# Kernel tuning notes

Hardware: AMD Instinct MI355X
Metric: run time of the kernel (lower is better)

Reference implementation:

```python
import jax, jax.numpy as jnp
import numpy as np

B, D, H1, H2 = 512, 1024, 512, 128

def setup_inputs() -> dict:
    key = jax.random.key(0)
    ks = jax.random.split(key, 3)
    x = jax.random.normal(ks[0], (B, D), dtype=jnp.float32)
    W1 = jax.random.normal(ks[1], (H1, D), dtype=jnp.float32)
    W2 = jax.random.normal(ks[2], (H2, H1), dtype=jnp.float32)
    b1 = jnp.full((H1,), 0.1, dtype=jnp.float32)
    b2 = jnp.full((H2,), 0.1, dtype=jnp.float32)
    b3 = jnp.full((H1,), 0.1, dtype=jnp.float32)
    b_r = jnp.full((D,), 0.1, dtype=jnp.float32)
    return {"x": x, "W1": W1, "b1": b1, "W2": W2, "b2": b2, "b3": b3, "b_r": b_r}

def reference(x, W1, b1, W2, b2, b3, b_r):
    # encoder
    c1 = jax.nn.sigmoid(x @ W1.T + b1)          # [B, H1]
    c2 = jax.nn.sigmoid(c1 @ W2.T + b2)         # [B, H2]
    # decoder (tied weights)
    c3 = jax.nn.sigmoid(c2 @ W2 + b3)           # [B, H1]
    recover = c3 @ W1 + b_r                     # [B, D]
    # Jacobian of code w.r.t. x, batched (replaces per-sample diag+matmul loop):
    # Jac[b] = diag(c2'(b)) @ W2 @ diag(c1'(b)) @ W1
    s1p = c1 * (1.0 - c1)                       # [B, H1]
    s2p = c2 * (1.0 - c2)                       # [B, H2]
    M = s2p[:, :, None] * W2[None, :, :] * s1p[:, None, :]   # [B, H2, H1]
    Jac = jnp.einsum('bhk,kd->bhd', M, W1)      # [B, H2, D]
    return (recover, c2, Jac)
```

## Files before the change

### kernel.cpp

```cpp
#include <hip/hip_runtime.h>


typedef _Float16 f16x8 __attribute__((ext_vector_type(8)));
typedef _Float16 f16x4 __attribute__((ext_vector_type(4)));
typedef float    f32x4 __attribute__((ext_vector_type(4)));
typedef float    f32x2 __attribute__((ext_vector_type(2)));

__device__ __forceinline__ void gld_lds16(const _Float16* src, _Float16* dst_wave_uniform) {
    __builtin_amdgcn_global_load_lds((const __attribute__((address_space(1))) unsigned int*)src,
                                     (__attribute__((address_space(3))) unsigned int*)dst_wave_uniform,
                                     16, 0, 0);
}

__global__ __launch_bounds__(256) void prep_kernel(const float* __restrict__ W1,
                                                   const float* __restrict__ W2,
                                                   _Float16* __restrict__ W1T,
                                                   _Float16* __restrict__ W2h) {
    int bx = blockIdx.x;
    if (bx < 512) {
        __shared__ float tile[32][33];
        int dt = (bx & 31) * 32, kt = (bx >> 5) * 32;
        int tx = threadIdx.x & 31, ty = threadIdx.x >> 5;
        #pragma unroll
        for (int r = 0; r < 32; r += 8)
            tile[ty + r][tx] = W1[(kt + ty + r) * 1024 + dt + tx];
        __syncthreads();
        #pragma unroll
        for (int r = 0; r < 32; r += 8)
            W1T[(size_t)(dt + ty + r) * 512 + kt + tx] = (_Float16)tile[tx][ty + r];
    } else {
        int i = (bx - 512) * 1024 + threadIdx.x * 4;
        f32x4 v = *(const f32x4*)(W2 + i);
        f16x4 h;
        h.x = (_Float16)v.x; h.y = (_Float16)v.y; h.z = (_Float16)v.z; h.w = (_Float16)v.w;
        *(f16x4*)(W2h + i) = h;
    }
}

template <int EPI, bool TRANSB>
__global__ __launch_bounds__(256) void gemm_f32(const float* __restrict__ A,
                                                const float* __restrict__ Bm,
                                                const float* __restrict__ bias,
                                                float* __restrict__ C,
                                                float* __restrict__ Cd,
                                                _Float16* __restrict__ Ch,
                                                int M, int N, int K) {
    __shared__ __align__(16) float As[16][34];
    __shared__ __align__(16) float Bs[16][68];
    const int n0 = blockIdx.x * 64, m0 = blockIdx.y * 32;
    const int tid = threadIdx.x, tx = tid & 15, ty = tid >> 4;
    float acc[2][4] = {};

    for (int k0 = 0; k0 < K; k0 += 16) {
        #pragma unroll
        for (int r = 0; r < 2; ++r) {
            int m = (tid >> 4) + r * 16, k = tid & 15;
            As[k][m] = A[(size_t)(m0 + m) * K + k0 + k];
        }
        if (TRANSB) {
            #pragma unroll
            for (int r = 0; r < 4; ++r) {
                int n = (tid >> 4) + r * 16, k = tid & 15;
                Bs[k][n] = Bm[(size_t)(n0 + n) * K + k0 + k];
            }
        } else {
            #pragma unroll
            for (int r = 0; r < 4; ++r) {
                int k = (tid >> 6) + r * 4, n = tid & 63;
                Bs[k][n] = Bm[(size_t)(k0 + k) * N + n0 + n];
            }
        }
        __syncthreads();
        #pragma unroll
        for (int k = 0; k < 16; ++k) {
            f32x2 av = *(const f32x2*)&As[k][ty * 2];
            f32x4 bv = *(const f32x4*)&Bs[k][tx * 4];
            #pragma unroll
            for (int i = 0; i < 2; ++i)
                #pragma unroll
                for (int j = 0; j < 4; ++j)
                    acc[i][j] += av[i] * bv[j];
        }
        __syncthreads();
    }

    #pragma unroll
    for (int i = 0; i < 2; ++i) {
        int row = m0 + ty * 2 + i;
        #pragma unroll
        for (int j = 0; j < 4; ++j) {
            int col = n0 + tx * 4 + j;
            float z = acc[i][j] + bias[col];
            float s = 1.f / (1.f + __expf(-z));
            if constexpr (EPI == 1) {
                C[(size_t)row * N + col]  = s;
                Cd[(size_t)row * N + col] = s * (1.f - s);
            } else {
                Ch[(size_t)row * N + col] = (_Float16)s;
            }
        }
    }
}

__global__ __launch_bounds__(256) void build_A(const float* __restrict__ W2,
                                               const float* __restrict__ s1p,
                                               const float* __restrict__ s2p,
                                               _Float16* __restrict__ A_all) {
    const int b = blockIdx.x, tid = threadIdx.x;
    __shared__ float S1[512];
    __shared__ float S2[128];
    S1[tid]       = s1p[(size_t)b * 512 + tid];
    S1[tid + 256] = s1p[(size_t)b * 512 + tid + 256];
    if (tid < 128) S2[tid] = s2p[(size_t)b * 128 + tid];
    __syncthreads();
    _Float16* out = A_all + (size_t)b * 65536;
    #pragma unroll 4
    for (int i = 0; i < 32; ++i) {
        int c = tid + 256 * i;
        int h = c >> 6, k8 = (c & 63) * 8;
        f32x4 w0 = *(const f32x4*)(W2 + h * 512 + k8);
        f32x4 w1 = *(const f32x4*)(W2 + h * 512 + k8 + 4);
        float s2 = S2[h];
        f16x8 o;
        o[0] = (_Float16)(s2 * w0.x * S1[k8 + 0]);
        o[1] = (_Float16)(s2 * w0.y * S1[k8 + 1]);
        o[2] = (_Float16)(s2 * w0.z * S1[k8 + 2]);
        o[3] = (_Float16)(s2 * w0.w * S1[k8 + 3]);
        o[4] = (_Float16)(s2 * w1.x * S1[k8 + 4]);
        o[5] = (_Float16)(s2 * w1.y * S1[k8 + 5]);
        o[6] = (_Float16)(s2 * w1.z * S1[k8 + 6]);
        o[7] = (_Float16)(s2 * w1.w * S1[k8 + 7]);
        *(f16x8*)(out + h * 512 + k8) = o;
    }
}

template <bool HAS_BIAS>
__global__ __launch_bounds__(256) void mfma_bt(const _Float16* __restrict__ Abase,
                                               const _Float16* __restrict__ Bmat,
                                               const float* __restrict__ bias,
                                               float* __restrict__ OutBase,
                                               int K, int N,
                                               long aBatch, long oBatch) {
    __shared__ __align__(16) _Float16 Asl[128 * 64];
    __shared__ __align__(16) _Float16 Bsl[128 * 64];
    __shared__ float Bias[128];
    const _Float16* A = Abase + (size_t)blockIdx.z * aBatch;
    float* Out = OutBase + (size_t)blockIdx.z * oBatch;
    const int m0 = blockIdx.y * 128, n0 = blockIdx.x * 128;
    const int tid = threadIdx.x;
    const int lane = tid & 63, wave = tid >> 6;
    const int wm = (wave >> 1) * 64, wn = (wave & 1) * 64;
    const int l15 = lane & 15, q = lane >> 4;

    if (HAS_BIAS && tid < 128) Bias[tid] = bias[n0 + tid];

    f32x4 acc[4][4];
    #pragma unroll
    for (int i = 0; i < 4; ++i)
        #pragma unroll
        for (int j = 0; j < 4; ++j) acc[i][j] = (f32x4){0.f, 0.f, 0.f, 0.f};

    const int rbase = wave * 8 + (lane >> 3);
    const int kof   = (lane & 7) * 8;

    for (int k0 = 0; k0 < K; k0 += 64) {
        #pragma unroll
        for (int r = 0; r < 4; ++r) {
            gld_lds16(A    + (size_t)(m0 + r * 32 + rbase) * K + k0 + kof, Asl + (r * 32 + wave * 8) * 64);
            gld_lds16(Bmat + (size_t)(n0 + r * 32 + rbase) * K + k0 + kof, Bsl + (r * 32 + wave * 8) * 64);
        }
        __syncthreads();
        #pragma unroll
        for (int kk = 0; kk < 64; kk += 32) {
            f16x8 af[4], bf[4];
            #pragma unroll
            for (int i = 0; i < 4; ++i)
                af[i] = *(const f16x8*)(Asl + (wm + i * 16 + l15) * 64 + kk + q * 8);
            #pragma unroll
            for (int j = 0; j < 4; ++j)
                bf[j] = *(const f16x8*)(Bsl + (wn + j * 16 + l15) * 64 + kk + q * 8);
            #pragma unroll
            for (int i = 0; i < 4; ++i)
                #pragma unroll
                for (int j = 0; j < 4; ++j)
                    acc[i][j] = __builtin_amdgcn_mfma_f32_16x16x32_f16(af[i], bf[j], acc[i][j], 0, 0, 0);
        }
        __syncthreads();
    }

    #pragma unroll
    for (int i = 0; i < 4; ++i) {
        #pragma unroll
        for (int rg = 0; rg < 4; ++rg) {
            int m = m0 + wm + i * 16 + q * 4 + rg;
            #pragma unroll
            for (int j = 0; j < 4; ++j) {
                int dcol = wn + j * 16 + l15;
                float v = acc[i][j][rg];
                if (HAS_BIAS) v += Bias[dcol];
                Out[(size_t)m * N + n0 + dcol] = v;
            }
        }
    }
}

__global__ __launch_bounds__(256) void jac_kernel(const _Float16* __restrict__ W2h,
                                                  const _Float16* __restrict__ W1T,
                                                  const float* __restrict__ s1p,
                                                  const float* __restrict__ s2p,
                                                  float* __restrict__ Jac) {
    __shared__ __align__(16) _Float16 Asl[128 * 64];
    __shared__ __align__(16) _Float16 Bsl[128 * 64];
    __shared__ float Ssl[128];
    const int b  = blockIdx.y;
    const int n0 = blockIdx.x * 128;
    const int tid = threadIdx.x;
    const int lane = tid & 63, wave = tid >> 6;
    const int wm = (wave >> 1) * 64, wn = (wave & 1) * 64;
    const int l15 = lane & 15, q = lane >> 4;

    if (tid < 128) Ssl[tid] = s2p[b * 128 + tid];

    f32x4 acc[4][4];
    #pragma unroll
    for (int i = 0; i < 4; ++i)
        #pragma unroll
        for (int j = 0; j < 4; ++j) acc[i][j] = (f32x4){0.f, 0.f, 0.f, 0.f};

    const int ah  = tid >> 4;
    const int akq = (tid & 15) * 4;
    const int rbase = wave * 8 + (lane >> 3);
    const int kof   = (lane & 7) * 8;

    for (int k0 = 0; k0 < 512; k0 += 64) {
        f32x4 s4 = *(const f32x4*)(s1p + (size_t)b * 512 + k0 + akq);
        f16x4 s4h;
        s4h.x = (_Float16)s4.x; s4h.y = (_Float16)s4.y;
        s4h.z = (_Float16)s4.z; s4h.w = (_Float16)s4.w;
        #pragma unroll
        for (int r = 0; r < 8; ++r) {
            int h = ah + r * 16;
            f16x4 w4 = *(const f16x4*)(W2h + (size_t)h * 512 + k0 + akq);
            *(f16x4*)(Asl + h * 64 + akq) = w4 * s4h;
        }
        #pragma unroll
        for (int r = 0; r < 4; ++r)
            gld_lds16(W1T + (size_t)(n0 + r * 32 + rbase) * 512 + k0 + kof,
                      Bsl + (r * 32 + wave * 8) * 64);
        __syncthreads();

        #pragma unroll
        for (int kk = 0; kk < 64; kk += 32) {
            f16x8 af[4], bf[4];
            #pragma unroll
            for (int i = 0; i < 4; ++i)
                af[i] = *(const f16x8*)(Asl + (wm + i * 16 + l15) * 64 + kk + q * 8);
            #pragma unroll
            for (int j = 0; j < 4; ++j)
                bf[j] = *(const f16x8*)(Bsl + (wn + j * 16 + l15) * 64 + kk + q * 8);
            #pragma unroll
            for (int i = 0; i < 4; ++i)
                #pragma unroll
                for (int j = 0; j < 4; ++j)
                    acc[i][j] = __builtin_amdgcn_mfma_f32_16x16x32_f16(af[i], bf[j], acc[i][j], 0, 0, 0);
        }
        __syncthreads();
    }

    float* outb = Jac + (size_t)b * (128 * 1024);
    #pragma unroll
    for (int i = 0; i < 4; ++i) {
        #pragma unroll
        for (int rg = 0; rg < 4; ++rg) {
            int h = wm + i * 16 + q * 4 + rg;
            float s = Ssl[h];
            #pragma unroll
            for (int j = 0; j < 4; ++j) {
                int d = n0 + wn + j * 16 + l15;
                outb[(size_t)h * 1024 + d] = acc[i][j][rg] * s;
            }
        }
    }
}

extern "C" void kernel_launch(void* const* d_in, const int* in_sizes, int n_in,
                              void* d_out, int out_size, void* d_ws, size_t ws_size,
                              hipStream_t stream) {
    const float* x  = (const float*)d_in[0];
    const float* W1 = (const float*)d_in[1];
    const float* b1 = (const float*)d_in[2];
    const float* W2 = (const float*)d_in[3];
    const float* b2 = (const float*)d_in[4];
    const float* b3 = (const float*)d_in[5];
    const float* br = (const float*)d_in[6];

    float* out_rec = (float*)d_out;
    float* out_c2  = out_rec + 512 * 1024;
    float* out_jac = out_c2 + 512 * 128;

    char* ws = (char*)d_ws;
    _Float16* W1T   = (_Float16*)(ws);
    _Float16* W2h   = (_Float16*)(ws + 0x100000);
    float*    c1    = (float*)(ws + 0x120000);
    float*    s1p   = (float*)(ws + 0x220000);
    float*    s2p   = (float*)(ws + 0x320000);
    _Float16* c3h   = (_Float16*)(ws + 0x360000);
    _Float16* A_all = (_Float16*)(ws + 0x400000);
    const bool big_ws = ws_size >= (size_t)0x4400000;

    prep_kernel<<<576, 256, 0, stream>>>(W1, W2, W1T, W2h);
    gemm_f32<1, true ><<<dim3(8, 16), 256, 0, stream>>>(x,      W1, b1, c1,     s1p, nullptr, 512, 512, 1024);
    gemm_f32<1, true ><<<dim3(2, 16), 256, 0, stream>>>(c1,     W2, b2, out_c2, s2p, nullptr, 512, 128, 512);
    gemm_f32<2, false><<<dim3(8, 16), 256, 0, stream>>>(out_c2, W2, b3, nullptr, nullptr, c3h, 512, 512, 128);
    mfma_bt<true><<<dim3(8, 4, 1), 256, 0, stream>>>(c3h, W1T, br, out_rec, 512, 1024, 0, 0);
    if (big_ws) {
        build_A<<<512, 256, 0, stream>>>(W2, s1p, s2p, A_all);
        mfma_bt<false><<<dim3(8, 1, 512), 256, 0, stream>>>(A_all, W1T, nullptr, out_jac,
                                                            512, 1024, 65536, 131072);
    } else {
        jac_kernel<<<dim3(8, 512), 256, 0, stream>>>(W2h, W1T, s1p, s2p, out_jac);
    }
}
```

Baseline: 459.8 us.

## Fuse independent stages into combined launches and register-prefetch fp32 GEMM tiles

Merges weight prep with the first encoder GEMM, the decoder GEMM with the Jacobian A-matrix build, and the reconstruction MFMA GEMM with the batched Jacobian GEMM into single launches that dispatch on block index. This cuts the launch count and lets independent work run concurrently. The fp32 GEMM now uses a K-tile of 32 and prefetches the next tile into registers while the current one is consumed. The Jacobian blocks are remapped so that consecutive blocks share W1T column tiles. The cost is that block roles within each launch are unbalanced, and register pressure rises from the prefetch.

```diff
diff --git a/kernel.cpp b/kernel.cpp
--- a/kernel.cpp
+++ b/kernel.cpp
@@ -12,11 +12,10 @@
                                      16, 0, 0);
 }
 
-__global__ __launch_bounds__(256) void prep_kernel(const float* __restrict__ W1,
-                                                   const float* __restrict__ W2,
-                                                   _Float16* __restrict__ W1T,
-                                                   _Float16* __restrict__ W2h) {
-    int bx = blockIdx.x;
+__device__ __forceinline__ void prep_dev(int bx, const float* __restrict__ W1,
+                                         const float* __restrict__ W2,
+                                         _Float16* __restrict__ W1T,
+                                         _Float16* __restrict__ W2h) {
     if (bx < 512) {
         __shared__ float tile[32][33];
         int dt = (bx & 31) * 32, kt = (bx >> 5) * 32;
@@ -38,41 +37,55 @@
 }
 
 template <int EPI, bool TRANSB>
-__global__ __launch_bounds__(256) void gemm_f32(const float* __restrict__ A,
-                                                const float* __restrict__ Bm,
-                                                const float* __restrict__ bias,
-                                                float* __restrict__ C,
-                                                float* __restrict__ Cd,
-                                                _Float16* __restrict__ Ch,
-                                                int M, int N, int K) {
-    __shared__ __align__(16) float As[16][34];
-    __shared__ __align__(16) float Bs[16][68];
-    const int n0 = blockIdx.x * 64, m0 = blockIdx.y * 32;
+__device__ void gemm_dev(const float* __restrict__ A, const float* __restrict__ Bm,
+                         const float* __restrict__ bias,
+                         float* __restrict__ C, float* __restrict__ Cd,
+                         _Float16* __restrict__ Ch,
+                         int M, int N, int K, int m0, int n0) {
+    __shared__ __align__(16) float As[32][34];
+    __shared__ __align__(16) float Bs[32][68];
     const int tid = threadIdx.x, tx = tid & 15, ty = tid >> 4;
+    const int ka  = tid & 31, ma  = tid >> 5;
+    const int kbt = tid & 31, nbt = tid >> 5;
+    const int nbf = tid & 63, kbf = tid >> 6;
     float acc[2][4] = {};
-
-    for (int k0 = 0; k0 < K; k0 += 16) {
-        #pragma unroll
-        for (int r = 0; r < 2; ++r) {
-            int m = (tid >> 4) + r * 16, k = tid & 15;
-            As[k][m] = A[(size_t)(m0 + m) * K + k0 + k];
-        }
+    float rA[4], rB[8];
+
+    #pragma unroll
+    for (int r = 0; r < 4; ++r) rA[r] = A[(size_t)(m0 + ma + 8 * r) * K + ka];
+    if (TRANSB) {
+        #pragma unroll
+        for (int r = 0; r < 8; ++r) rB[r] = Bm[(size_t)(n0 + nbt + 8 * r) * K + kbt];
+    } else {
+        #pragma unroll
+        for (int r = 0; r < 8; ++r) rB[r] = Bm[(size_t)(kbf + 4 * r) * N + n0 + nbf];
+    }
+
+    for (int k0 = 0; k0 < K; k0 += 32) {
+        #pragma unroll
+        for (int r = 0; r < 4; ++r) As[ka][ma + 8 * r] = rA[r];
         if (TRANSB) {
             #pragma unroll
-            for (int r = 0; r < 4; ++r) {
-                int n = (tid >> 4) + r * 16, k = tid & 15;
-                Bs[k][n] = Bm[(size_t)(n0 + n) * K + k0 + k];
+            for (int r = 0; r < 8; ++r) Bs[kbt][nbt + 8 * r] = rB[r];
+        } else {
+            #pragma unroll
+            for (int r = 0; r < 8; ++r) Bs[kbf + 4 * r][nbf] = rB[r];
+        }
+        const int k1 = k0 + 32;
+        if (k1 < K) {
+            #pragma unroll
+            for (int r = 0; r < 4; ++r) rA[r] = A[(size_t)(m0 + ma + 8 * r) * K + k1 + ka];
+            if (TRANSB) {
+                #pragma unroll
+                for (int r = 0; r < 8; ++r) rB[r] = Bm[(size_t)(n0 + nbt + 8 * r) * K + k1 + kbt];
+            } else {
+                #pragma unroll
+                for (int r = 0; r < 8; ++r) rB[r] = Bm[(size_t)(k1 + kbf + 4 * r) * N + n0 + nbf];
             }
-        } else {
-            #pragma unroll
-            for (int r = 0; r < 4; ++r) {
-                int k = (tid >> 6) + r * 4, n = tid & 63;
-                Bs[k][n] = Bm[(size_t)(k0 + k) * N + n0 + n];
-            }
-        }
-        __syncthreads();
-        #pragma unroll
-        for (int k = 0; k < 16; ++k) {
+        }
+        __syncthreads();
+        #pragma unroll
+        for (int k = 0; k < 32; ++k) {
             f32x2 av = *(const f32x2*)&As[k][ty * 2];
             f32x4 bv = *(const f32x4*)&Bs[k][tx * 4];
             #pragma unroll
@@ -102,11 +115,11 @@
     }
 }
 
-__global__ __launch_bounds__(256) void build_A(const float* __restrict__ W2,
-                                               const float* __restrict__ s1p,
-                                               const float* __restrict__ s2p,
-                                               _Float16* __restrict__ A_all) {
-    const int b = blockIdx.x, tid = threadIdx.x;
+__device__ __forceinline__ void buildA_dev(int b, const float* __restrict__ W2,
+                                           const float* __restrict__ s1p,
+                                           const float* __restrict__ s2p,
+                                           _Float16* __restrict__ A_all) {
+    const int tid = threadIdx.x;
     __shared__ float S1[512];
     __shared__ float S2[128];
     S1[tid]       = s1p[(size_t)b * 512 + tid];
@@ -134,6 +147,140 @@
     }
 }
 
+__global__ __launch_bounds__(256) void fused_prep_gemm1(const float* __restrict__ x,
+                                                        const float* __restrict__ W1,
+                                                        const float* __restrict__ b1,
+                                                        const float* __restrict__ W2,
+                                                        _Float16* __restrict__ W1T,
+                                                        _Float16* __restrict__ W2h,
+                                                        float* __restrict__ c1,
+                                                        float* __restrict__ s1p) {
+    int bx = blockIdx.x;
+    if (bx < 128) {
+        gemm_dev<1, true>(x, W1, b1, c1, s1p, nullptr, 512, 512, 1024,
+                          (bx >> 3) * 32, (bx & 7) * 64);
+    } else {
+        prep_dev(bx - 128, W1, W2, W1T, W2h);
+    }
+}
+
+__global__ __launch_bounds__(256) void gemm2_kernel(const float* __restrict__ c1,
+                                                    const float* __restrict__ W2,
+                                                    const float* __restrict__ b2,
+                                                    float* __restrict__ out_c2,
+                                                    float* __restrict__ s2p) {
+    gemm_dev<1, true>(c1, W2, b2, out_c2, s2p, nullptr, 512, 128, 512,
+                      blockIdx.y * 32, blockIdx.x * 64);
+}
+
+__global__ __launch_bounds__(256) void gemm3_kernel(const float* __restrict__ out_c2,
+                                                    const float* __restrict__ W2,
+                                                    const float* __restrict__ b3,
+                                                    _Float16* __restrict__ c3h) {
+    gemm_dev<2, false>(out_c2, W2, b3, nullptr, nullptr, c3h, 512, 512, 128,
+                       (blockIdx.x >> 3) * 32, (blockIdx.x & 7) * 64);
+}
+
+__global__ __launch_bounds__(256) void fused_mid(const float* __restrict__ out_c2,
+                                                 const float* __restrict__ W2,
+                                                 const float* __restrict__ b3,
+                                                 _Float16* __restrict__ c3h,
+                                                 const float* __restrict__ s1p,
+                                                 const float* __restrict__ s2p,
+                                                 _Float16* __restrict__ A_all) {
+    int bx = blockIdx.x;
+    if (bx < 128) {
+        gemm_dev<2, false>(out_c2, W2, b3, nullptr, nullptr, c3h, 512, 512, 128,
+                           (bx >> 3) * 32, (bx & 7) * 64);
+    } else {
+        buildA_dev(bx - 128, W2, s1p, s2p, A_all);
+    }
+}
+
+__global__ __launch_bounds__(256) void fused_mfma(const _Float16* __restrict__ c3h,
+                                                  const _Float16* __restrict__ A_all,
+                                                  const _Float16* __restrict__ W1T,
+                                                  const float* __restrict__ br,
+                                                  float* __restrict__ out_rec,
+                                                  float* __restrict__ out_jac) {
+    __shared__ __align__(16) _Float16 Asl[128 * 64];
+    __shared__ __align__(16) _Float16 Bsl[128 * 64];
+    __shared__ float Bias[128];
+
+    const int bid = blockIdx.x;
+    const _Float16* A;
+    float* Out;
+    int m0, n0;
+    bool has_bias;
+    if (bid < 32) {
+        has_bias = true;
+        A = c3h; Out = out_rec;
+        n0 = (bid & 7) * 128; m0 = (bid >> 3) * 128;
+    } else {
+        int jid = bid - 32;
+        int w = (jid & 7) * 512 + (jid >> 3);
+        int z = w >> 3;
+        has_bias = false;
+        A = A_all + (size_t)z * 65536;
+        Out = out_jac + (size_t)z * 131072;
+        n0 = (w & 7) * 128; m0 = 0;
+    }
+    const int K = 512, Nn = 1024;
+    const int tid = threadIdx.x;
+    const int lane = tid & 63, wave = tid >> 6;
+    const int wm = (wave >> 1) * 64, wn = (wave & 1) * 64;
+    const int l15 = lane & 15, q = lane >> 4;
+
+    if (tid < 128) Bias[tid] = has_bias ? br[n0 + tid] : 0.f;
+
+    f32x4 acc[4][4];
+    #pragma unroll
+    for (int i = 0; i < 4; ++i)
+        #pragma unroll
+        for (int j = 0; j < 4; ++j) acc[i][j] = (f32x4){0.f, 0.f, 0.f, 0.f};
+
+    const int rbase = wave * 8 + (lane >> 3);
+    const int kof   = (lane & 7) * 8;
+
+    for (int k0 = 0; k0 < K; k0 += 64) {
+        #pragma unroll
+        for (int r = 0; r < 4; ++r) {
+            gld_lds16(A   + (size_t)(m0 + r * 32 + rbase) * K + k0 + kof, Asl + (r * 32 + wave * 8) * 64);
+            gld_lds16(W1T + (size_t)(n0 + r * 32 + rbase) * K + k0 + kof, Bsl + (r * 32 + wave * 8) * 64);
+        }
+        __syncthreads();
+        #pragma unroll
+        for (int kk = 0; kk < 64; kk += 32) {
+            f16x8 af[4], bf[4];
+            #pragma unroll
+            for (int i = 0; i < 4; ++i)
+                af[i] = *(const f16x8*)(Asl + (wm + i * 16 + l15) * 64 + kk + q * 8);
+            #pragma unroll
+            for (int j = 0; j < 4; ++j)
+                bf[j] = *(const f16x8*)(Bsl + (wn + j * 16 + l15) * 64 + kk + q * 8);
+            #pragma unroll
+            for (int i = 0; i < 4; ++i)
+                #pragma unroll
+                for (int j = 0; j < 4; ++j)
+                    acc[i][j] = __builtin_amdgcn_mfma_f32_16x16x32_f16(af[i], bf[j], acc[i][j], 0, 0, 0);
+        }
+        __syncthreads();
+    }
+
+    #pragma unroll
+    for (int i = 0; i < 4; ++i) {
+        #pragma unroll
+        for (int rg = 0; rg < 4; ++rg) {
+            int m = m0 + wm + i * 16 + q * 4 + rg;
+            #pragma unroll
+            for (int j = 0; j < 4; ++j) {
+                int dcol = wn + j * 16 + l15;
+                Out[(size_t)m * Nn + n0 + dcol] = acc[i][j][rg] + Bias[dcol];
+            }
+        }
+    }
+}
+
 template <bool HAS_BIAS>
 __global__ __launch_bounds__(256) void mfma_bt(const _Float16* __restrict__ Abase,
                                                const _Float16* __restrict__ Bmat,
@@ -308,16 +455,14 @@
     _Float16* A_all = (_Float16*)(ws + 0x400000);
     const bool big_ws = ws_size >= (size_t)0x4400000;
 
-    prep_kernel<<<576, 256, 0, stream>>>(W1, W2, W1T, W2h);
-    gemm_f32<1, true ><<<dim3(8, 16), 256, 0, stream>>>(x,      W1, b1, c1,     s1p, nullptr, 512, 512, 1024);
-    gemm_f32<1, true ><<<dim3(2, 16), 256, 0, stream>>>(c1,     W2, b2, out_c2, s2p, nullptr, 512, 128, 512);
-    gemm_f32<2, false><<<dim3(8, 16), 256, 0, stream>>>(out_c2, W2, b3, nullptr, nullptr, c3h, 512, 512, 128);
-    mfma_bt<true><<<dim3(8, 4, 1), 256, 0, stream>>>(c3h, W1T, br, out_rec, 512, 1024, 0, 0);
+    fused_prep_gemm1<<<704, 256, 0, stream>>>(x, W1, b1, W2, W1T, W2h, c1, s1p);
+    gemm2_kernel<<<dim3(2, 16), 256, 0, stream>>>(c1, W2, b2, out_c2, s2p);
     if (big_ws) {
-        build_A<<<512, 256, 0, stream>>>(W2, s1p, s2p, A_all);
-        mfma_bt<false><<<dim3(8, 1, 512), 256, 0, stream>>>(A_all, W1T, nullptr, out_jac,
-                                                            512, 1024, 65536, 131072);
-    } else {
+        fused_mid<<<640, 256, 0, stream>>>(out_c2, W2, b3, c3h, s1p, s2p, A_all);
+        fused_mfma<<<4128, 256, 0, stream>>>(c3h, A_all, W1T, br, out_rec, out_jac);
+    } else {
+        gemm3_kernel<<<128, 256, 0, stream>>>(out_c2, W2, b3, c3h);
+        mfma_bt<true><<<dim3(8, 4, 1), 256, 0, stream>>>(c3h, W1T, br, out_rec, 512, 1024, 0, 0);
         jac_kernel<<<dim3(8, 512), 256, 0, stream>>>(W2h, W1T, s1p, s2p, out_jac);
     }
 }
```

Measured after the change: 436.1 us. 5.2% less time.
